# Kernel optimization log

Hardware: AMD Instinct MI355X
Metric: run time of the kernel (lower is better)

Reference implementation:

```python
import jax, jax.numpy as jnp
import numpy as np

B, N, C, H = 8, 1024, 768, 12
D = C // H
SCALE = D ** -0.5


def setup_inputs() -> dict:
    key = jax.random.key(0)
    ks = jax.random.split(key, 6)
    std = 0.02
    return {
        "x": jax.random.normal(ks[0], (B, N, C), dtype=jnp.float32),
        "w_qkv": jax.random.normal(ks[1], (3 * C, C), dtype=jnp.float32) * std,
        "w_proj": jax.random.normal(ks[2], (C, C), dtype=jnp.float32) * std,
        "b_proj": jnp.zeros((C,), dtype=jnp.float32),
        "conv_l_w": jax.random.normal(ks[3], (H, H), dtype=jnp.float32) * std,
        "conv_w_w": jax.random.normal(ks[4], (H, H), dtype=jnp.float32) * std,
    }


def reference(x, w_qkv, w_proj, b_proj, conv_l_w, conv_w_w):
    Bx, Nx, Cx = x.shape
    # qkv projection: torch Linear uses x @ W^T
    qkv = (x @ w_qkv.T).reshape(Bx, Nx, 3, H, D)
    qkv = jnp.transpose(qkv, (2, 0, 3, 1, 4))  # [3, B, H, N, D]
    q, k, v = qkv[0], qkv[1], qkv[2]
    q = q * SCALE
    attn = jnp.einsum("bhnd,bhmd->bhnm", q, k)  # [B,H,N,N]
    # 1x1 conv across heads (conv_l)
    attn = jnp.einsum("oh,bhnm->bonm", conv_l_w, attn)
    attn = jax.nn.softmax(attn, axis=-1)
    # 1x1 conv across heads (conv_w)
    attn = jnp.einsum("oh,bhnm->bonm", conv_w_w, attn)
    out = jnp.einsum("bhnm,bhmd->bhnd", attn, v)
    out = jnp.transpose(out, (0, 2, 1, 3)).reshape(Bx, Nx, Cx)
    return out @ w_proj.T + b_proj
```

## Files before the change

kernel.cpp:

```cpp
#include <hip/hip_runtime.h>
#include <hip/hip_bf16.h>

typedef __attribute__((ext_vector_type(8))) short short8;
typedef __attribute__((ext_vector_type(4))) short short4v;
typedef __attribute__((ext_vector_type(4))) float float4v;

#define NB 8
#define NH 12
#define NN 1024
#define ND 64
#define NC 768

#define RAWBAR() do { \
  asm volatile("s_waitcnt lgkmcnt(0)" ::: "memory"); \
  __builtin_amdgcn_s_barrier(); \
} while (0)

__device__ __forceinline__ short f2bf(float f) {
  __hip_bfloat16 h = __float2bfloat16(f);
  union { __hip_bfloat16 h; short s; } u; u.h = h; return u.s;
}
__device__ __forceinline__ unsigned pk2(float a, float b) {
  unsigned ua = (unsigned short)f2bf(a);
  unsigned ub = (unsigned short)f2bf(b);
  return ua | (ub << 16);
}

template<int MODE>
__global__ __launch_bounds__(256, 2)
void gemm_kernel(const void* __restrict__ Ap, const float* __restrict__ Bw,
                 const float* __restrict__ bias,
                 __hip_bfloat16* __restrict__ Qo, __hip_bfloat16* __restrict__ Ko,
                 __hip_bfloat16* __restrict__ VTo, float* __restrict__ Out)
{
  __shared__ short As[128 * 40];
  __shared__ short Bs[128 * 40];
  const int tid = threadIdx.x;
  const int w = tid >> 6, lane = tid & 63, lr = lane & 15, lg = lane >> 4;
  const int wr = w >> 1, wc = w & 1;
  const int n0 = blockIdx.x * 128, m0 = blockIdx.y * 128;

  float4v acc[4][4];
  #pragma unroll
  for (int i = 0; i < 4; i++)
    #pragma unroll
    for (int j = 0; j < 4; j++)
      acc[i][j] = (float4v){0.f, 0.f, 0.f, 0.f};

  for (int kt = 0; kt < 768; kt += 32) {
    if (MODE == 0) {
      const float* A = (const float*)Ap;
      #pragma unroll
      for (int i2 = 0; i2 < 4; i2++) {
        int c = tid + 256 * i2;
        int row = c >> 3, c4 = c & 7;
        float4v v = *(const float4v*)(A + (size_t)(m0 + row) * 768 + kt + c4 * 4);
        short4v s = { f2bf(v[0]), f2bf(v[1]), f2bf(v[2]), f2bf(v[3]) };
        *(short4v*)(&As[row * 40 + c4 * 4]) = s;
      }
    } else {
      const __hip_bfloat16* A = (const __hip_bfloat16*)Ap;
      #pragma unroll
      for (int i2 = 0; i2 < 2; i2++) {
        int c = tid + 256 * i2;
        int row = c >> 2, c8 = c & 3;
        *(short8*)(&As[row * 40 + c8 * 8]) =
            *(const short8*)(A + (size_t)(m0 + row) * 768 + kt + c8 * 8);
      }
    }
    #pragma unroll
    for (int i2 = 0; i2 < 4; i2++) {
      int c = tid + 256 * i2;
      int row = c >> 3, c4 = c & 7;
      float4v v = *(const float4v*)(Bw + (size_t)(n0 + row) * 768 + kt + c4 * 4);
      short4v s = { f2bf(v[0]), f2bf(v[1]), f2bf(v[2]), f2bf(v[3]) };
      *(short4v*)(&Bs[row * 40 + c4 * 4]) = s;
    }
    __syncthreads();

    short8 af[4], bfr[4];
    #pragma unroll
    for (int i = 0; i < 4; i++)
      af[i] = *(const short8*)(&As[(wr * 64 + i * 16 + lr) * 40 + lg * 8]);
    #pragma unroll
    for (int j = 0; j < 4; j++)
      bfr[j] = *(const short8*)(&Bs[(wc * 64 + j * 16 + lr) * 40 + lg * 8]);
    #pragma unroll
    for (int i = 0; i < 4; i++)
      #pragma unroll
      for (int j = 0; j < 4; j++)
        acc[i][j] = __builtin_amdgcn_mfma_f32_16x16x32_bf16(af[i], bfr[j], acc[i][j], 0, 0, 0);
    __syncthreads();
  }

  #pragma unroll
  for (int i = 0; i < 4; i++) {
    #pragma unroll
    for (int j = 0; j < 4; j++) {
      #pragma unroll
      for (int r = 0; r < 4; r++) {
        float val = acc[i][j][r];
        int mg_ = m0 + wr * 64 + i * 16 + lg * 4 + r;
        int ng_ = n0 + wc * 64 + j * 16 + lr;
        if (MODE == 0) {
          int s = ng_ / 768;
          int rem = ng_ - s * 768;
          int h = rem >> 6, d = rem & 63;
          int b = mg_ >> 10, n = mg_ & 1023;
          if (s == 0)
            Qo[(((size_t)b * NH + h) * NN + n) * ND + d] = __float2bfloat16(val * 0.125f);
          else if (s == 1)
            Ko[(((size_t)b * NH + h) * NN + n) * ND + d] = __float2bfloat16(val);
          else
            VTo[(((size_t)b * NH + h) * ND + d) * NN + n] = __float2bfloat16(val);
        } else {
          Out[(size_t)mg_ * NC + ng_] = val + bias[ng_];
        }
      }
    }
  }
}

__global__ __launch_bounds__(256, 2)
void attn_kernel(const __hip_bfloat16* __restrict__ Qg, const __hip_bfloat16* __restrict__ Kg,
                 const __hip_bfloat16* __restrict__ VTg,
                 const float* __restrict__ convl, const float* __restrict__ convw,
                 __hip_bfloat16* __restrict__ AOut)
{
  __shared__ short Sb[32 * 576];
  __shared__ short pm[16 * 648];
  __shared__ short lwA[512];
  __shared__ short wwT[512];

  const int tid = threadIdx.x;
  const int w = tid >> 6, lane = tid & 63, lr = lane & 15, lg = lane >> 4;
  const int b = blockIdx.x & 7;
  const int n0 = (blockIdx.x >> 3) * 16;
  const float4v zf = (float4v){0.f, 0.f, 0.f, 0.f};

  for (int i = tid; i < 512; i += 256) {
    int r = i >> 5, k = i & 31;
    bool v = (r < 12) && (k < 12);
    lwA[i] = v ? f2bf(convl[r * 12 + k]) : (short)0;
    wwT[i] = v ? f2bf(convw[r * 12 + k]) : (short)0;
  }
  for (int i = tid; i < 512; i += 256) {
    short* p = &Sb[i * 36 + 12];
    #pragma unroll
    for (int j = 0; j < 24; j++) p[j] = 0;
  }

  short8 qf[3][2];
  #pragma unroll
  for (int hh = 0; hh < 3; hh++)
    #pragma unroll
    for (int ks = 0; ks < 2; ks++)
      qf[hh][ks] = *(const short8*)(Qg +
          (((size_t)b * NH + w * 3 + hh) * NN + n0 + lr) * ND + ks * 32 + lg * 8);

  short8 kreg[3][2][2];
  auto loadK = [&](int t) {
    const int m0t = t * 32;
    #pragma unroll
    for (int hh = 0; hh < 3; hh++) {
      const size_t kbase = (((size_t)b * NH + w * 3 + hh) * NN + m0t) * ND;
      #pragma unroll
      for (int j = 0; j < 2; j++)
        #pragma unroll
        for (int ks = 0; ks < 2; ks++)
          kreg[hh][j][ks] = *(const short8*)(Kg + kbase +
              (size_t)(j * 16 + lr) * ND + ks * 32 + lg * 8);
    }
  };
  short8 vt[3][4];
  auto loadVT = [&](int t) {
    const int m0v = t * 32;
    #pragma unroll
    for (int hh = 0; hh < 3; hh++) {
      const size_t vbase = ((size_t)b * NH + w * 3 + hh) * ND * NN;
      #pragma unroll
      for (int jd = 0; jd < 4; jd++)
        vt[hh][jd] = *(const short8*)(VTg + vbase +
            (size_t)(jd * 16 + lr) * NN + m0v + lg * 8);
    }
  };

  loadK(0);
  RAWBAR();
  const short8 lwf = *(const short8*)(&lwA[lr * 32 + lg * 8]);
  const short8 wwf = *(const short8*)(&wwT[lr * 32 + lg * 8]);

  float Lacc[4][4];
  #pragma unroll
  for (int r = 0; r < 4; r++)
    #pragma unroll
    for (int nn = 0; nn < 4; nn++) Lacc[r][nn] = 0.f;

  for (int t = 0; t < 32; t++) {
    __builtin_amdgcn_s_setprio(1);
    #pragma unroll
    for (int hh = 0; hh < 3; hh++) {
      const int h = w * 3 + hh;
      #pragma unroll
      for (int j = 0; j < 2; j++) {
        float4v a = zf;
        #pragma unroll
        for (int ks = 0; ks < 2; ks++)
          a = __builtin_amdgcn_mfma_f32_16x16x32_bf16(qf[hh][ks], kreg[hh][j][ks], a, 0, 0, 0);
        #pragma unroll
        for (int r = 0; r < 4; r++)
          Sb[((lg * 4 + r) * 2 + j) * 576 + lr * 36 + h] = f2bf(a[r]);
      }
    }
    __builtin_amdgcn_s_setprio(0);
    loadK(t < 31 ? t + 1 : 0);
    RAWBAR();
    #pragma unroll
    for (int cc = 0; cc < 8; cc++) {
      const int c = w * 8 + cc;
      short8 sb = *(const short8*)(&Sb[c * 576 + lr * 36 + lg * 8]);
      float4v d = __builtin_amdgcn_mfma_f32_16x16x32_bf16(lwf, sb, zf, 0, 0, 0);
      #pragma unroll
      for (int r = 0; r < 4; r++)
        Lacc[r][cc >> 1] += __expf(d[r]);
    }
    RAWBAR();
  }
  float logLreg[4][4];
  #pragma unroll
  for (int r = 0; r < 4; r++)
    #pragma unroll
    for (int nn = 0; nn < 4; nn++) {
      float v = Lacc[r][nn];
      v += __shfl_xor(v, 1);
      v += __shfl_xor(v, 2);
      v += __shfl_xor(v, 4);
      v += __shfl_xor(v, 8);
      logLreg[r][nn] = __logf(v);
    }

  float4v oacc[3][4];
  #pragma unroll
  for (int hh = 0; hh < 3; hh++)
    #pragma unroll
    for (int jd = 0; jd < 4; jd++) oacc[hh][jd] = zf;

  for (int t = 0; t <= 32; t++) {
    short8 pf[3];
    if (t > 0) {
      #pragma unroll
      for (int hh = 0; hh < 3; hh++)
        pf[hh] = *(const short8*)(&pm[(w * 3 + hh) * 648 + lr * 40 + lg * 8]);
    }
    __builtin_amdgcn_s_setprio(1);
    if (t < 32) {
      #pragma unroll
      for (int hh = 0; hh < 3; hh++) {
        const int h = w * 3 + hh;
        #pragma unroll
        for (int j = 0; j < 2; j++) {
          float4v a = zf;
          #pragma unroll
          for (int ks = 0; ks < 2; ks++)
            a = __builtin_amdgcn_mfma_f32_16x16x32_bf16(qf[hh][ks], kreg[hh][j][ks], a, 0, 0, 0);
          #pragma unroll
          for (int r = 0; r < 4; r++)
            Sb[((lg * 4 + r) * 2 + j) * 576 + lr * 36 + h] = f2bf(a[r]);
        }
      }
      if (t < 31) loadK(t + 1);
    }
    if (t > 0) {
      #pragma unroll
      for (int hh = 0; hh < 3; hh++)
        #pragma unroll
        for (int jd = 0; jd < 4; jd++)
          oacc[hh][jd] = __builtin_amdgcn_mfma_f32_16x16x32_bf16(vt[hh][jd], pf[hh], oacc[hh][jd], 0, 0, 0);
    }
    __builtin_amdgcn_s_setprio(0);
    RAWBAR();
    if (t < 32) {
      loadVT(t);
      #pragma unroll
      for (int cc = 0; cc < 8; cc++) {
        const int c = w * 8 + cc;
        short8 sb = *(const short8*)(&Sb[c * 576 + lr * 36 + lg * 8]);
        float4v d = __builtin_amdgcn_mfma_f32_16x16x32_bf16(lwf, sb, zf, 0, 0, 0);
        float p0 = __expf(d[0] - logLreg[0][cc >> 1]);
        float p1 = __expf(d[1] - logLreg[1][cc >> 1]);
        float p2 = __expf(d[2] - logLreg[2][cc >> 1]);
        float p3 = __expf(d[3] - logLreg[3][cc >> 1]);
        unsigned* dst = (unsigned*)(&Sb[c * 576 + lr * 36 + lg * 4]);
        dst[0] = pk2(p0, p1);
        dst[1] = pk2(p2, p3);
      }
      asm volatile("s_waitcnt lgkmcnt(0)" ::: "memory");
      __builtin_amdgcn_sched_barrier(0);
      #pragma unroll
      for (int cc = 0; cc < 8; cc++) {
        const int c = w * 8 + cc;
        short8 pb = *(const short8*)(&Sb[c * 576 + lr * 36 + lg * 8]);
        float4v d = __builtin_amdgcn_mfma_f32_16x16x32_bf16(pb, wwf, zf, 0, 0, 0);
        unsigned* dst = (unsigned*)(&pm[lr * 648 + (c >> 1) * 40 + (c & 1) * 16 + lg * 4]);
        dst[0] = pk2(d[0], d[1]);
        dst[1] = pk2(d[2], d[3]);
      }
    }
    RAWBAR();
  }

  #pragma unroll
  for (int hh = 0; hh < 3; hh++) {
    const int o2 = w * 3 + hh;
    #pragma unroll
    for (int jd = 0; jd < 4; jd++) {
      size_t base = ((size_t)b * NN + n0 + lr) * NC + o2 * 64 + jd * 16 + lg * 4;
      unsigned* dst = (unsigned*)(&AOut[base]);
      dst[0] = pk2(oacc[hh][jd][0], oacc[hh][jd][1]);
      dst[1] = pk2(oacc[hh][jd][2], oacc[hh][jd][3]);
    }
  }
}

extern "C" void kernel_launch(void* const* d_in, const int* in_sizes, int n_in,
                              void* d_out, int out_size, void* d_ws, size_t ws_size,
                              hipStream_t stream) {
  const float* x      = (const float*)d_in[0];
  const float* w_qkv  = (const float*)d_in[1];
  const float* w_proj = (const float*)d_in[2];
  const float* b_proj = (const float*)d_in[3];
  const float* conv_l = (const float*)d_in[4];
  const float* conv_w = (const float*)d_in[5];
  float* out = (float*)d_out;

  const size_t NE = (size_t)NB * NH * NN * ND;
  __hip_bfloat16* Qb = (__hip_bfloat16*)d_ws;
  __hip_bfloat16* Kb = Qb + NE;
  __hip_bfloat16* VT = Kb + NE;
  __hip_bfloat16* AO = VT + NE;

  gemm_kernel<0><<<dim3(18, 64), 256, 0, stream>>>(x, w_qkv, nullptr, Qb, Kb, VT, nullptr);
  attn_kernel<<<dim3(512), 256, 0, stream>>>(Qb, Kb, VT, conv_l, conv_w, AO);
  gemm_kernel<1><<<dim3(6, 64), 256, 0, stream>>>(AO, w_proj, b_proj, nullptr, nullptr, nullptr, out);
}
```

Measured before the change: 375.5 us.

## Split attention work across 8 waves and swizzle score buffer in LDS

The attention kernel grows from 4 to 8 wavefronts per block. Each wave now owns three (head, key-half) units instead of three whole heads, which halves per-wave registers for K, V^T and the output accumulators. The padded score buffer becomes a compact 32-byte-stride layout with an XOR swizzle to avoid LDS bank conflicts, shrinking LDS use. V^T loads move into the consumer step and are issued right before use. More waves should improve latency hiding, at the cost of more barrier participants and V loads that are no longer prefetched a step ahead.

```diff
diff --git a/kernel.cpp b/kernel.cpp
--- a/kernel.cpp
+++ b/kernel.cpp
@@ -15,6 +15,8 @@
   asm volatile("s_waitcnt lgkmcnt(0)" ::: "memory"); \
   __builtin_amdgcn_s_barrier(); \
 } while (0)
+
+#define SWZ(byt) ((byt) ^ (((((byt) >> 5) ^ ((byt) >> 12)) & 7) << 4))
 
 __device__ __forceinline__ short f2bf(float f) {
   __hip_bfloat16 h = __float2bfloat16(f);
@@ -121,67 +123,56 @@
   }
 }
 
-__global__ __launch_bounds__(256, 2)
+__global__ __launch_bounds__(512, 4)
 void attn_kernel(const __hip_bfloat16* __restrict__ Qg, const __hip_bfloat16* __restrict__ Kg,
                  const __hip_bfloat16* __restrict__ VTg,
                  const float* __restrict__ convl, const float* __restrict__ convw,
                  __hip_bfloat16* __restrict__ AOut)
 {
-  __shared__ short Sb[32 * 576];
+  __shared__ short Sb[8256];
   __shared__ short pm[16 * 648];
   __shared__ short lwA[512];
   __shared__ short wwT[512];
 
+  char* Sbb = (char*)Sb;
   const int tid = threadIdx.x;
   const int w = tid >> 6, lane = tid & 63, lr = lane & 15, lg = lane >> 4;
   const int b = blockIdx.x & 7;
   const int n0 = (blockIdx.x >> 3) * 16;
+  const int u0 = w * 3;
+  const int h0 = u0 >> 1;
   const float4v zf = (float4v){0.f, 0.f, 0.f, 0.f};
 
-  for (int i = tid; i < 512; i += 256) {
+  for (int i = tid; i < 512; i += 512) {
     int r = i >> 5, k = i & 31;
     bool v = (r < 12) && (k < 12);
     lwA[i] = v ? f2bf(convl[r * 12 + k]) : (short)0;
     wwT[i] = v ? f2bf(convw[r * 12 + k]) : (short)0;
   }
-  for (int i = tid; i < 512; i += 256) {
-    short* p = &Sb[i * 36 + 12];
-    #pragma unroll
-    for (int j = 0; j < 24; j++) p[j] = 0;
-  }
-
-  short8 qf[3][2];
-  #pragma unroll
-  for (int hh = 0; hh < 3; hh++)
+  {
+    int chunk = tid >> 4, col = tid & 15;
+    *(int*)(Sbb + SWZ(chunk * 512 + col * 32 + 24)) = 0;
+    *(int*)(Sbb + SWZ(chunk * 512 + col * 32 + 28)) = 0;
+    if (tid < 32) *(int*)(Sbb + 16384 + tid * 4) = 0;
+  }
+
+  short8 qf[2][2];
+  #pragma unroll
+  for (int hi = 0; hi < 2; hi++)
     #pragma unroll
     for (int ks = 0; ks < 2; ks++)
-      qf[hh][ks] = *(const short8*)(Qg +
-          (((size_t)b * NH + w * 3 + hh) * NN + n0 + lr) * ND + ks * 32 + lg * 8);
-
-  short8 kreg[3][2][2];
+      qf[hi][ks] = *(const short8*)(Qg +
+          (((size_t)b * NH + h0 + hi) * NN + n0 + lr) * ND + ks * 32 + lg * 8);
+
+  short8 kreg[3][2];
   auto loadK = [&](int t) {
-    const int m0t = t * 32;
-    #pragma unroll
-    for (int hh = 0; hh < 3; hh++) {
-      const size_t kbase = (((size_t)b * NH + w * 3 + hh) * NN + m0t) * ND;
-      #pragma unroll
-      for (int j = 0; j < 2; j++)
-        #pragma unroll
-        for (int ks = 0; ks < 2; ks++)
-          kreg[hh][j][ks] = *(const short8*)(Kg + kbase +
-              (size_t)(j * 16 + lr) * ND + ks * 32 + lg * 8);
-    }
-  };
-  short8 vt[3][4];
-  auto loadVT = [&](int t) {
-    const int m0v = t * 32;
-    #pragma unroll
-    for (int hh = 0; hh < 3; hh++) {
-      const size_t vbase = ((size_t)b * NH + w * 3 + hh) * ND * NN;
-      #pragma unroll
-      for (int jd = 0; jd < 4; jd++)
-        vt[hh][jd] = *(const short8*)(VTg + vbase +
-            (size_t)(jd * 16 + lr) * NN + m0v + lg * 8);
+    #pragma unroll
+    for (int uu = 0; uu < 3; uu++) {
+      int u = u0 + uu, h = u >> 1, j = u & 1;
+      const size_t kbase = (((size_t)b * NH + h) * NN + t * 32 + j * 16 + lr) * ND;
+      #pragma unroll
+      for (int ks = 0; ks < 2; ks++)
+        kreg[uu][ks] = *(const short8*)(Kg + kbase + ks * 32 + lg * 8);
     }
   };
 
@@ -190,35 +181,28 @@
   const short8 lwf = *(const short8*)(&lwA[lr * 32 + lg * 8]);
   const short8 wwf = *(const short8*)(&wwT[lr * 32 + lg * 8]);
 
-  float Lacc[4][4];
-  #pragma unroll
-  for (int r = 0; r < 4; r++)
-    #pragma unroll
-    for (int nn = 0; nn < 4; nn++) Lacc[r][nn] = 0.f;
+  float Lacc[4][2];
+  #pragma unroll
+  for (int r = 0; r < 4; r++) { Lacc[r][0] = 0.f; Lacc[r][1] = 0.f; }
 
   for (int t = 0; t < 32; t++) {
     __builtin_amdgcn_s_setprio(1);
     #pragma unroll
-    for (int hh = 0; hh < 3; hh++) {
-      const int h = w * 3 + hh;
-      #pragma unroll
-      for (int j = 0; j < 2; j++) {
-        float4v a = zf;
-        #pragma unroll
-        for (int ks = 0; ks < 2; ks++)
-          a = __builtin_amdgcn_mfma_f32_16x16x32_bf16(qf[hh][ks], kreg[hh][j][ks], a, 0, 0, 0);
-        #pragma unroll
-        for (int r = 0; r < 4; r++)
-          Sb[((lg * 4 + r) * 2 + j) * 576 + lr * 36 + h] = f2bf(a[r]);
-      }
+    for (int uu = 0; uu < 3; uu++) {
+      int u = u0 + uu, h = u >> 1, j = u & 1, hi = h - h0;
+      float4v a = __builtin_amdgcn_mfma_f32_16x16x32_bf16(qf[hi][0], kreg[uu][0], zf, 0, 0, 0);
+      a = __builtin_amdgcn_mfma_f32_16x16x32_bf16(qf[hi][1], kreg[uu][1], a, 0, 0, 0);
+      #pragma unroll
+      for (int r = 0; r < 4; r++)
+        *(short*)(Sbb + SWZ((((lg * 4 + r) * 2 + j) * 512) + lr * 32 + h * 2)) = f2bf(a[r]);
     }
     __builtin_amdgcn_s_setprio(0);
     loadK(t < 31 ? t + 1 : 0);
     RAWBAR();
     #pragma unroll
-    for (int cc = 0; cc < 8; cc++) {
-      const int c = w * 8 + cc;
-      short8 sb = *(const short8*)(&Sb[c * 576 + lr * 36 + lg * 8]);
+    for (int cc = 0; cc < 4; cc++) {
+      const int c = w * 4 + cc;
+      short8 sb = *(const short8*)(Sbb + SWZ(c * 512 + lr * 32 + lg * 16));
       float4v d = __builtin_amdgcn_mfma_f32_16x16x32_bf16(lwf, sb, zf, 0, 0, 0);
       #pragma unroll
       for (int r = 0; r < 4; r++)
@@ -226,11 +210,11 @@
     }
     RAWBAR();
   }
-  float logLreg[4][4];
+  float logLreg[4][2];
   #pragma unroll
   for (int r = 0; r < 4; r++)
     #pragma unroll
-    for (int nn = 0; nn < 4; nn++) {
+    for (int nn = 0; nn < 2; nn++) {
       float v = Lacc[r][nn];
       v += __shfl_xor(v, 1);
       v += __shfl_xor(v, 2);
@@ -239,67 +223,67 @@
       logLreg[r][nn] = __logf(v);
     }
 
-  float4v oacc[3][4];
-  #pragma unroll
-  for (int hh = 0; hh < 3; hh++)
-    #pragma unroll
-    for (int jd = 0; jd < 4; jd++) oacc[hh][jd] = zf;
+  float4v oacc[3][2];
+  #pragma unroll
+  for (int uu = 0; uu < 3; uu++) { oacc[uu][0] = zf; oacc[uu][1] = zf; }
 
   for (int t = 0; t <= 32; t++) {
     short8 pf[3];
+    short8 vt[3][2];
     if (t > 0) {
-      #pragma unroll
-      for (int hh = 0; hh < 3; hh++)
-        pf[hh] = *(const short8*)(&pm[(w * 3 + hh) * 648 + lr * 40 + lg * 8]);
+      const int m0v = (t - 1) * 32;
+      #pragma unroll
+      for (int uu = 0; uu < 3; uu++) {
+        int u = u0 + uu, o2v = u >> 1, jdp = u & 1;
+        pf[uu] = *(const short8*)(&pm[o2v * 648 + lr * 40 + lg * 8]);
+        const size_t vbase = ((size_t)b * NH + o2v) * ND * NN;
+        #pragma unroll
+        for (int q = 0; q < 2; q++)
+          vt[uu][q] = *(const short8*)(VTg + vbase +
+              (size_t)((jdp * 2 + q) * 16 + lr) * NN + m0v + lg * 8);
+      }
     }
     __builtin_amdgcn_s_setprio(1);
     if (t < 32) {
       #pragma unroll
-      for (int hh = 0; hh < 3; hh++) {
-        const int h = w * 3 + hh;
+      for (int uu = 0; uu < 3; uu++) {
+        int u = u0 + uu, h = u >> 1, j = u & 1, hi = h - h0;
+        float4v a = __builtin_amdgcn_mfma_f32_16x16x32_bf16(qf[hi][0], kreg[uu][0], zf, 0, 0, 0);
+        a = __builtin_amdgcn_mfma_f32_16x16x32_bf16(qf[hi][1], kreg[uu][1], a, 0, 0, 0);
         #pragma unroll
-        for (int j = 0; j < 2; j++) {
-          float4v a = zf;
-          #pragma unroll
-          for (int ks = 0; ks < 2; ks++)
-            a = __builtin_amdgcn_mfma_f32_16x16x32_bf16(qf[hh][ks], kreg[hh][j][ks], a, 0, 0, 0);
-          #pragma unroll
-          for (int r = 0; r < 4; r++)
-            Sb[((lg * 4 + r) * 2 + j) * 576 + lr * 36 + h] = f2bf(a[r]);
-        }
+        for (int r = 0; r < 4; r++)
+          *(short*)(Sbb + SWZ((((lg * 4 + r) * 2 + j) * 512) + lr * 32 + h * 2)) = f2bf(a[r]);
       }
       if (t < 31) loadK(t + 1);
     }
     if (t > 0) {
       #pragma unroll
-      for (int hh = 0; hh < 3; hh++)
+      for (int uu = 0; uu < 3; uu++)
         #pragma unroll
-        for (int jd = 0; jd < 4; jd++)
-          oacc[hh][jd] = __builtin_amdgcn_mfma_f32_16x16x32_bf16(vt[hh][jd], pf[hh], oacc[hh][jd], 0, 0, 0);
+        for (int q = 0; q < 2; q++)
+          oacc[uu][q] = __builtin_amdgcn_mfma_f32_16x16x32_bf16(vt[uu][q], pf[uu], oacc[uu][q], 0, 0, 0);
     }
     __builtin_amdgcn_s_setprio(0);
     RAWBAR();
     if (t < 32) {
-      loadVT(t);
-      #pragma unroll
-      for (int cc = 0; cc < 8; cc++) {
-        const int c = w * 8 + cc;
-        short8 sb = *(const short8*)(&Sb[c * 576 + lr * 36 + lg * 8]);
+      #pragma unroll
+      for (int cc = 0; cc < 4; cc++) {
+        const int c = w * 4 + cc;
+        short8 sb = *(const short8*)(Sbb + SWZ(c * 512 + lr * 32 + lg * 16));
         float4v d = __builtin_amdgcn_mfma_f32_16x16x32_bf16(lwf, sb, zf, 0, 0, 0);
         float p0 = __expf(d[0] - logLreg[0][cc >> 1]);
         float p1 = __expf(d[1] - logLreg[1][cc >> 1]);
         float p2 = __expf(d[2] - logLreg[2][cc >> 1]);
         float p3 = __expf(d[3] - logLreg[3][cc >> 1]);
-        unsigned* dst = (unsigned*)(&Sb[c * 576 + lr * 36 + lg * 4]);
-        dst[0] = pk2(p0, p1);
-        dst[1] = pk2(p2, p3);
+        *(unsigned*)(Sbb + SWZ(c * 512 + lr * 32 + lg * 8)) = pk2(p0, p1);
+        *(unsigned*)(Sbb + SWZ(c * 512 + lr * 32 + lg * 8 + 4)) = pk2(p2, p3);
       }
       asm volatile("s_waitcnt lgkmcnt(0)" ::: "memory");
       __builtin_amdgcn_sched_barrier(0);
       #pragma unroll
-      for (int cc = 0; cc < 8; cc++) {
-        const int c = w * 8 + cc;
-        short8 pb = *(const short8*)(&Sb[c * 576 + lr * 36 + lg * 8]);
+      for (int cc = 0; cc < 4; cc++) {
+        const int c = w * 4 + cc;
+        short8 pb = *(const short8*)(Sbb + SWZ(c * 512 + lr * 32 + lg * 16));
         float4v d = __builtin_amdgcn_mfma_f32_16x16x32_bf16(pb, wwf, zf, 0, 0, 0);
         unsigned* dst = (unsigned*)(&pm[lr * 648 + (c >> 1) * 40 + (c & 1) * 16 + lg * 4]);
         dst[0] = pk2(d[0], d[1]);
@@ -310,14 +294,14 @@
   }
 
   #pragma unroll
-  for (int hh = 0; hh < 3; hh++) {
-    const int o2 = w * 3 + hh;
-    #pragma unroll
-    for (int jd = 0; jd < 4; jd++) {
-      size_t base = ((size_t)b * NN + n0 + lr) * NC + o2 * 64 + jd * 16 + lg * 4;
+  for (int uu = 0; uu < 3; uu++) {
+    int u = u0 + uu, o2v = u >> 1, jdp = u & 1;
+    #pragma unroll
+    for (int q = 0; q < 2; q++) {
+      size_t base = ((size_t)b * NN + n0 + lr) * NC + o2v * 64 + jdp * 32 + q * 16 + lg * 4;
       unsigned* dst = (unsigned*)(&AOut[base]);
-      dst[0] = pk2(oacc[hh][jd][0], oacc[hh][jd][1]);
-      dst[1] = pk2(oacc[hh][jd][2], oacc[hh][jd][3]);
+      dst[0] = pk2(oacc[uu][q][0], oacc[uu][q][1]);
+      dst[1] = pk2(oacc[uu][q][2], oacc[uu][q][3]);
     }
   }
 }
@@ -340,6 +324,6 @@
   __hip_bfloat16* AO = VT + NE;
 
   gemm_kernel<0><<<dim3(18, 64), 256, 0, stream>>>(x, w_qkv, nullptr, Qb, Kb, VT, nullptr);
-  attn_kernel<<<dim3(512), 256, 0, stream>>>(Qb, Kb, VT, conv_l, conv_w, AO);
+  attn_kernel<<<dim3(512), 512, 0, stream>>>(Qb, Kb, VT, conv_l, conv_w, AO);
   gemm_kernel<1><<<dim3(6, 64), 256, 0, stream>>>(AO, w_proj, b_proj, nullptr, nullptr, nullptr, out);
 }
```

New measurement: 674.9 us. +79.7%, slower.

## Double-buffer score and probability LDS tiles to drop one barrier per step

Applied to the files above, without the earlier changes.

Sb and pm become double-buffered with tighter strides (18 and 584/36 instead of 36 and 648/40). QK^T for tile t is written to one buffer while the conv/exp work for tile t-1 reads the other. This removes one of the two barriers per iteration and deepens the pipeline to three stages, with the PV MFMA lagging two tiles. V^T loads move next to the PV step, and LDS use grows, which may limit the 2-blocks-per-CU occupancy target.

```diff
diff --git a/kernel.cpp b/kernel.cpp
--- a/kernel.cpp
+++ b/kernel.cpp
@@ -127,8 +127,8 @@
                  const float* __restrict__ convl, const float* __restrict__ convw,
                  __hip_bfloat16* __restrict__ AOut)
 {
-  __shared__ short Sb[32 * 576];
-  __shared__ short pm[16 * 648];
+  __shared__ short Sb[18432];
+  __shared__ short pm[18688];
   __shared__ short lwA[512];
   __shared__ short wwT[512];
 
@@ -144,10 +144,9 @@
     lwA[i] = v ? f2bf(convl[r * 12 + k]) : (short)0;
     wwT[i] = v ? f2bf(convw[r * 12 + k]) : (short)0;
   }
-  for (int i = tid; i < 512; i += 256) {
-    short* p = &Sb[i * 36 + 12];
-    #pragma unroll
-    for (int j = 0; j < 24; j++) p[j] = 0;
+  for (int i = tid; i < 1024; i += 256) {
+    unsigned* p = (unsigned*)(&Sb[i * 18 + 12]);
+    p[0] = 0; p[1] = 0; p[2] = 0;
   }
 
   short8 qf[3][2];
@@ -160,10 +159,9 @@
 
   short8 kreg[3][2][2];
   auto loadK = [&](int t) {
-    const int m0t = t * 32;
     #pragma unroll
     for (int hh = 0; hh < 3; hh++) {
-      const size_t kbase = (((size_t)b * NH + w * 3 + hh) * NN + m0t) * ND;
+      const size_t kbase = (((size_t)b * NH + w * 3 + hh) * NN + t * 32) * ND;
       #pragma unroll
       for (int j = 0; j < 2; j++)
         #pragma unroll
@@ -172,16 +170,19 @@
               (size_t)(j * 16 + lr) * ND + ks * 32 + lg * 8);
     }
   };
-  short8 vt[3][4];
-  auto loadVT = [&](int t) {
-    const int m0v = t * 32;
+
+  auto qkStep = [&](int buf) {
     #pragma unroll
     for (int hh = 0; hh < 3; hh++) {
-      const size_t vbase = ((size_t)b * NH + w * 3 + hh) * ND * NN;
-      #pragma unroll
-      for (int jd = 0; jd < 4; jd++)
-        vt[hh][jd] = *(const short8*)(VTg + vbase +
-            (size_t)(jd * 16 + lr) * NN + m0v + lg * 8);
+      const int h = w * 3 + hh;
+      #pragma unroll
+      for (int j = 0; j < 2; j++) {
+        float4v a = __builtin_amdgcn_mfma_f32_16x16x32_bf16(qf[hh][0], kreg[hh][j][0], zf, 0, 0, 0);
+        a = __builtin_amdgcn_mfma_f32_16x16x32_bf16(qf[hh][1], kreg[hh][j][1], a, 0, 0, 0);
+        #pragma unroll
+        for (int r = 0; r < 4; r++)
+          Sb[(buf * 32 + (lg * 4 + r) * 2 + j) * 288 + lr * 18 + h] = f2bf(a[r]);
+      }
     }
   };
 
@@ -196,33 +197,22 @@
     #pragma unroll
     for (int nn = 0; nn < 4; nn++) Lacc[r][nn] = 0.f;
 
-  for (int t = 0; t < 32; t++) {
+  for (int t = 0; t <= 32; t++) {
     __builtin_amdgcn_s_setprio(1);
-    #pragma unroll
-    for (int hh = 0; hh < 3; hh++) {
-      const int h = w * 3 + hh;
-      #pragma unroll
-      for (int j = 0; j < 2; j++) {
-        float4v a = zf;
-        #pragma unroll
-        for (int ks = 0; ks < 2; ks++)
-          a = __builtin_amdgcn_mfma_f32_16x16x32_bf16(qf[hh][ks], kreg[hh][j][ks], a, 0, 0, 0);
+    if (t < 32) qkStep(t & 1);
+    __builtin_amdgcn_s_setprio(0);
+    if (t < 32) loadK(t < 31 ? t + 1 : 0);
+    if (t >= 1) {
+      const int buf = (t - 1) & 1;
+      #pragma unroll
+      for (int cc = 0; cc < 8; cc++) {
+        const int c = w * 8 + cc;
+        short8 sb = *(const short8*)(&Sb[(buf * 32 + c) * 288 + lr * 18 + lg * 8]);
+        float4v d = __builtin_amdgcn_mfma_f32_16x16x32_bf16(lwf, sb, zf, 0, 0, 0);
         #pragma unroll
         for (int r = 0; r < 4; r++)
-          Sb[((lg * 4 + r) * 2 + j) * 576 + lr * 36 + h] = f2bf(a[r]);
-      }
-    }
-    __builtin_amdgcn_s_setprio(0);
-    loadK(t < 31 ? t + 1 : 0);
-    RAWBAR();
-    #pragma unroll
-    for (int cc = 0; cc < 8; cc++) {
-      const int c = w * 8 + cc;
-      short8 sb = *(const short8*)(&Sb[c * 576 + lr * 36 + lg * 8]);
-      float4v d = __builtin_amdgcn_mfma_f32_16x16x32_bf16(lwf, sb, zf, 0, 0, 0);
-      #pragma unroll
-      for (int r = 0; r < 4; r++)
-        Lacc[r][cc >> 1] += __expf(d[r]);
+          Lacc[r][cc >> 1] += __expf(d[r]);
+      }
     }
     RAWBAR();
   }
@@ -245,52 +235,41 @@
     #pragma unroll
     for (int jd = 0; jd < 4; jd++) oacc[hh][jd] = zf;
 
-  for (int t = 0; t <= 32; t++) {
+  for (int t = 0; t <= 33; t++) {
     short8 pf[3];
-    if (t > 0) {
-      #pragma unroll
-      for (int hh = 0; hh < 3; hh++)
-        pf[hh] = *(const short8*)(&pm[(w * 3 + hh) * 648 + lr * 40 + lg * 8]);
+    short8 vt[3][4];
+    if (t >= 2) {
+      const int pb = t & 1;
+      const int m0v = (t - 2) * 32;
+      #pragma unroll
+      for (int hh = 0; hh < 3; hh++) {
+        const int o2 = w * 3 + hh;
+        pf[hh] = *(const short8*)(&pm[pb * 9344 + o2 * 584 + lr * 36 + lg * 8]);
+        const size_t vbase = ((size_t)b * NH + o2) * ND * NN;
+        #pragma unroll
+        for (int jd = 0; jd < 4; jd++)
+          vt[hh][jd] = *(const short8*)(VTg + vbase +
+              (size_t)(jd * 16 + lr) * NN + m0v + lg * 8);
+      }
     }
     __builtin_amdgcn_s_setprio(1);
     if (t < 32) {
-      #pragma unroll
-      for (int hh = 0; hh < 3; hh++) {
-        const int h = w * 3 + hh;
-        #pragma unroll
-        for (int j = 0; j < 2; j++) {
-          float4v a = zf;
-          #pragma unroll
-          for (int ks = 0; ks < 2; ks++)
-            a = __builtin_amdgcn_mfma_f32_16x16x32_bf16(qf[hh][ks], kreg[hh][j][ks], a, 0, 0, 0);
-          #pragma unroll
-          for (int r = 0; r < 4; r++)
-            Sb[((lg * 4 + r) * 2 + j) * 576 + lr * 36 + h] = f2bf(a[r]);
-        }
-      }
+      qkStep(t & 1);
       if (t < 31) loadK(t + 1);
     }
-    if (t > 0) {
-      #pragma unroll
-      for (int hh = 0; hh < 3; hh++)
-        #pragma unroll
-        for (int jd = 0; jd < 4; jd++)
-          oacc[hh][jd] = __builtin_amdgcn_mfma_f32_16x16x32_bf16(vt[hh][jd], pf[hh], oacc[hh][jd], 0, 0, 0);
-    }
     __builtin_amdgcn_s_setprio(0);
-    RAWBAR();
-    if (t < 32) {
-      loadVT(t);
+    if (t >= 1 && t <= 32) {
+      const int buf = (t - 1) & 1;
       #pragma unroll
       for (int cc = 0; cc < 8; cc++) {
         const int c = w * 8 + cc;
-        short8 sb = *(const short8*)(&Sb[c * 576 + lr * 36 + lg * 8]);
+        short8 sb = *(const short8*)(&Sb[(buf * 32 + c) * 288 + lr * 18 + lg * 8]);
         float4v d = __builtin_amdgcn_mfma_f32_16x16x32_bf16(lwf, sb, zf, 0, 0, 0);
         float p0 = __expf(d[0] - logLreg[0][cc >> 1]);
         float p1 = __expf(d[1] - logLreg[1][cc >> 1]);
         float p2 = __expf(d[2] - logLreg[2][cc >> 1]);
         float p3 = __expf(d[3] - logLreg[3][cc >> 1]);
-        unsigned* dst = (unsigned*)(&Sb[c * 576 + lr * 36 + lg * 4]);
+        unsigned* dst = (unsigned*)(&Sb[(buf * 32 + c) * 288 + lr * 18 + lg * 4]);
         dst[0] = pk2(p0, p1);
         dst[1] = pk2(p2, p3);
       }
@@ -299,12 +278,21 @@
       #pragma unroll
       for (int cc = 0; cc < 8; cc++) {
         const int c = w * 8 + cc;
-        short8 pb = *(const short8*)(&Sb[c * 576 + lr * 36 + lg * 8]);
-        float4v d = __builtin_amdgcn_mfma_f32_16x16x32_bf16(pb, wwf, zf, 0, 0, 0);
-        unsigned* dst = (unsigned*)(&pm[lr * 648 + (c >> 1) * 40 + (c & 1) * 16 + lg * 4]);
+        short8 pb2 = *(const short8*)(&Sb[(buf * 32 + c) * 288 + lr * 18 + lg * 8]);
+        float4v d = __builtin_amdgcn_mfma_f32_16x16x32_bf16(pb2, wwf, zf, 0, 0, 0);
+        unsigned* dst = (unsigned*)(&pm[buf * 9344 + lr * 584 + (c >> 1) * 36 + (c & 1) * 16 + lg * 4]);
         dst[0] = pk2(d[0], d[1]);
         dst[1] = pk2(d[2], d[3]);
       }
+    }
+    if (t >= 2) {
+      __builtin_amdgcn_s_setprio(1);
+      #pragma unroll
+      for (int hh = 0; hh < 3; hh++)
+        #pragma unroll
+        for (int jd = 0; jd < 4; jd++)
+          oacc[hh][jd] = __builtin_amdgcn_mfma_f32_16x16x32_bf16(vt[hh][jd], pf[hh], oacc[hh][jd], 0, 0, 0);
+      __builtin_amdgcn_s_setprio(0);
     }
     RAWBAR();
   }
```

New measurement: 377.0 us. No clear change (+0.4%).

## Split attention into L-sum and PV kernels with key-dimension halving

Applied to the files above, without the earlier changes.

The fused attention kernel becomes two kernels plus a reduction. The first computes the softmax denominators and the second the probability-times-V products, each splitting the key range into two halves so the grid doubles to 1024 blocks. Each block streams K/V straight from global memory instead of prefetching into registers, and shared-memory padding is reduced to raise occupancy. A separate add kernel sums the two partial outputs and writes them in token-major layout. The cost is recomputing QK^T in both passes, extra global traffic for the partial outputs, and two additional launches.

```diff
diff --git a/kernel.cpp b/kernel.cpp
--- a/kernel.cpp
+++ b/kernel.cpp
@@ -19,6 +19,9 @@
 __device__ __forceinline__ short f2bf(float f) {
   __hip_bfloat16 h = __float2bfloat16(f);
   union { __hip_bfloat16 h; short s; } u; u.h = h; return u.s;
+}
+__device__ __forceinline__ float bf2f(short s) {
+  union { float f; unsigned u; } u; u.u = ((unsigned)(unsigned short)s) << 16; return u.f;
 }
 __device__ __forceinline__ unsigned pk2(float a, float b) {
   unsigned ua = (unsigned short)f2bf(a);
@@ -121,34 +124,25 @@
   }
 }
 
-__global__ __launch_bounds__(256, 2)
-void attn_kernel(const __hip_bfloat16* __restrict__ Qg, const __hip_bfloat16* __restrict__ Kg,
-                 const __hip_bfloat16* __restrict__ VTg,
-                 const float* __restrict__ convl, const float* __restrict__ convw,
-                 __hip_bfloat16* __restrict__ AOut)
+__global__ __launch_bounds__(256, 4)
+void attn_l_kernel(const __hip_bfloat16* __restrict__ Qg, const __hip_bfloat16* __restrict__ Kg,
+                   const float* __restrict__ convl, float* __restrict__ Lg)
 {
-  __shared__ short Sb[32 * 576];
-  __shared__ short pm[16 * 648];
+  __shared__ short Sb[2 * 9408];
   __shared__ short lwA[512];
-  __shared__ short wwT[512];
-
   const int tid = threadIdx.x;
   const int w = tid >> 6, lane = tid & 63, lr = lane & 15, lg = lane >> 4;
   const int b = blockIdx.x & 7;
-  const int n0 = (blockIdx.x >> 3) * 16;
+  const int rest = blockIdx.x >> 3;
+  const int n0 = (rest >> 1) * 16;
+  const int mh = rest & 1;
   const float4v zf = (float4v){0.f, 0.f, 0.f, 0.f};
 
   for (int i = tid; i < 512; i += 256) {
     int r = i >> 5, k = i & 31;
-    bool v = (r < 12) && (k < 12);
-    lwA[i] = v ? f2bf(convl[r * 12 + k]) : (short)0;
-    wwT[i] = v ? f2bf(convw[r * 12 + k]) : (short)0;
-  }
-  for (int i = tid; i < 512; i += 256) {
-    short* p = &Sb[i * 36 + 12];
-    #pragma unroll
-    for (int j = 0; j < 24; j++) p[j] = 0;
-  }
+    lwA[i] = (r < 12 && k < 12) ? f2bf(convl[r * 12 + k]) : (short)0;
+  }
+  for (int i = tid; i < 9408; i += 256) ((unsigned*)Sb)[i] = 0u;
 
   short8 qf[3][2];
   #pragma unroll
@@ -157,38 +151,8 @@
     for (int ks = 0; ks < 2; ks++)
       qf[hh][ks] = *(const short8*)(Qg +
           (((size_t)b * NH + w * 3 + hh) * NN + n0 + lr) * ND + ks * 32 + lg * 8);
-
-  short8 kreg[3][2][2];
-  auto loadK = [&](int t) {
-    const int m0t = t * 32;
-    #pragma unroll
-    for (int hh = 0; hh < 3; hh++) {
-      const size_t kbase = (((size_t)b * NH + w * 3 + hh) * NN + m0t) * ND;
-      #pragma unroll
-      for (int j = 0; j < 2; j++)
-        #pragma unroll
-        for (int ks = 0; ks < 2; ks++)
-          kreg[hh][j][ks] = *(const short8*)(Kg + kbase +
-              (size_t)(j * 16 + lr) * ND + ks * 32 + lg * 8);
-    }
-  };
-  short8 vt[3][4];
-  auto loadVT = [&](int t) {
-    const int m0v = t * 32;
-    #pragma unroll
-    for (int hh = 0; hh < 3; hh++) {
-      const size_t vbase = ((size_t)b * NH + w * 3 + hh) * ND * NN;
-      #pragma unroll
-      for (int jd = 0; jd < 4; jd++)
-        vt[hh][jd] = *(const short8*)(VTg + vbase +
-            (size_t)(jd * 16 + lr) * NN + m0v + lg * 8);
-    }
-  };
-
-  loadK(0);
   RAWBAR();
   const short8 lwf = *(const short8*)(&lwA[lr * 32 + lg * 8]);
-  const short8 wwf = *(const short8*)(&wwT[lr * 32 + lg * 8]);
 
   float Lacc[4][4];
   #pragma unroll
@@ -196,37 +160,43 @@
     #pragma unroll
     for (int nn = 0; nn < 4; nn++) Lacc[r][nn] = 0.f;
 
-  for (int t = 0; t < 32; t++) {
+  for (int t = 0; t <= 16; t++) {
     __builtin_amdgcn_s_setprio(1);
-    #pragma unroll
-    for (int hh = 0; hh < 3; hh++) {
-      const int h = w * 3 + hh;
-      #pragma unroll
-      for (int j = 0; j < 2; j++) {
-        float4v a = zf;
+    if (t < 16) {
+      const int m0t = (mh * 16 + t) * 32;
+      const int buf = (t & 1) * 9408;
+      #pragma unroll
+      for (int hh = 0; hh < 3; hh++) {
+        const int h = w * 3 + hh;
+        const size_t kbase = (((size_t)b * NH + h) * NN + m0t) * ND;
         #pragma unroll
-        for (int ks = 0; ks < 2; ks++)
-          a = __builtin_amdgcn_mfma_f32_16x16x32_bf16(qf[hh][ks], kreg[hh][j][ks], a, 0, 0, 0);
+        for (int j = 0; j < 2; j++) {
+          short8 kb0 = *(const short8*)(Kg + kbase + (size_t)(j * 16 + lr) * ND + lg * 8);
+          short8 kb1 = *(const short8*)(Kg + kbase + (size_t)(j * 16 + lr) * ND + 32 + lg * 8);
+          float4v a = __builtin_amdgcn_mfma_f32_16x16x32_bf16(qf[hh][0], kb0, zf, 0, 0, 0);
+          a = __builtin_amdgcn_mfma_f32_16x16x32_bf16(qf[hh][1], kb1, a, 0, 0, 0);
+          #pragma unroll
+          for (int r = 0; r < 4; r++)
+            Sb[buf + ((lg * 4 + r) * 2 + j) * 292 + lr * 18 + h] = f2bf(a[r]);
+        }
+      }
+    }
+    __builtin_amdgcn_s_setprio(0);
+    if (t >= 1) {
+      const int buf = ((t - 1) & 1) * 9408;
+      #pragma unroll
+      for (int cc = 0; cc < 8; cc++) {
+        const int c = w * 8 + cc;
+        short8 sb = *(const short8*)(&Sb[buf + c * 292 + lr * 18 + lg * 8]);
+        float4v d = __builtin_amdgcn_mfma_f32_16x16x32_bf16(lwf, sb, zf, 0, 0, 0);
         #pragma unroll
         for (int r = 0; r < 4; r++)
-          Sb[((lg * 4 + r) * 2 + j) * 576 + lr * 36 + h] = f2bf(a[r]);
-      }
-    }
-    __builtin_amdgcn_s_setprio(0);
-    loadK(t < 31 ? t + 1 : 0);
+          Lacc[r][cc >> 1] += __expf(d[r]);
+      }
+    }
     RAWBAR();
-    #pragma unroll
-    for (int cc = 0; cc < 8; cc++) {
-      const int c = w * 8 + cc;
-      short8 sb = *(const short8*)(&Sb[c * 576 + lr * 36 + lg * 8]);
-      float4v d = __builtin_amdgcn_mfma_f32_16x16x32_bf16(lwf, sb, zf, 0, 0, 0);
-      #pragma unroll
-      for (int r = 0; r < 4; r++)
-        Lacc[r][cc >> 1] += __expf(d[r]);
-    }
-    RAWBAR();
-  }
-  float logLreg[4][4];
+  }
+
   #pragma unroll
   for (int r = 0; r < 4; r++)
     #pragma unroll
@@ -236,8 +206,64 @@
       v += __shfl_xor(v, 2);
       v += __shfl_xor(v, 4);
       v += __shfl_xor(v, 8);
-      logLreg[r][nn] = __logf(v);
-    }
+      int o = lg * 4 + r;
+      if (lr == 0 && o < 12)
+        Lg[((size_t)(mh * 8 + b) * NH + o) * NN + n0 + w * 4 + nn] = v;
+    }
+}
+
+__global__ __launch_bounds__(256, 3)
+void attn_pv_kernel(const __hip_bfloat16* __restrict__ Qg, const __hip_bfloat16* __restrict__ Kg,
+                    const __hip_bfloat16* __restrict__ VTg,
+                    const float* __restrict__ convl, const float* __restrict__ convw,
+                    const float* __restrict__ Lg, __hip_bfloat16* __restrict__ Ug)
+{
+  __shared__ short Sb[9408];
+  __shared__ short pm[9344];
+  __shared__ short lwA[512];
+  __shared__ short wwT[512];
+  __shared__ float invLs[256];
+
+  const int tid = threadIdx.x;
+  const int w = tid >> 6, lane = tid & 63, lr = lane & 15, lg = lane >> 4;
+  const int b = blockIdx.x & 7;
+  const int rest = blockIdx.x >> 3;
+  const int n0 = (rest >> 1) * 16;
+  const int mh = rest & 1;
+  const float4v zf = (float4v){0.f, 0.f, 0.f, 0.f};
+
+  for (int i = tid; i < 512; i += 256) {
+    int r = i >> 5, k = i & 31;
+    bool v = (r < 12) && (k < 12);
+    lwA[i] = v ? f2bf(convl[r * 12 + k]) : (short)0;
+    wwT[i] = v ? f2bf(convw[r * 12 + k]) : (short)0;
+  }
+  for (int i = tid; i < 4704; i += 256) ((unsigned*)Sb)[i] = 0u;
+  if (tid < 192) {
+    int o = tid >> 4, nl = tid & 15;
+    float l = Lg[((size_t)b * NH + o) * NN + n0 + nl] +
+              Lg[((size_t)(8 + b) * NH + o) * NN + n0 + nl];
+    invLs[tid] = 1.0f / l;
+  } else if (tid < 256) {
+    invLs[tid] = 0.f;
+  }
+
+  short8 qf[3][2];
+  #pragma unroll
+  for (int hh = 0; hh < 3; hh++)
+    #pragma unroll
+    for (int ks = 0; ks < 2; ks++)
+      qf[hh][ks] = *(const short8*)(Qg +
+          (((size_t)b * NH + w * 3 + hh) * NN + n0 + lr) * ND + ks * 32 + lg * 8);
+  RAWBAR();
+  const short8 lwf = *(const short8*)(&lwA[lr * 32 + lg * 8]);
+  const short8 wwf = *(const short8*)(&wwT[lr * 32 + lg * 8]);
+  float invLreg[4][4];
+  #pragma unroll
+  for (int r = 0; r < 4; r++)
+    #pragma unroll
+    for (int nn = 0; nn < 4; nn++)
+      invLreg[r][nn] = invLs[(lg * 4 + r) * 16 + w * 4 + nn];
 
   float4v oacc[3][4];
   #pragma unroll
@@ -245,52 +271,59 @@
     #pragma unroll
     for (int jd = 0; jd < 4; jd++) oacc[hh][jd] = zf;
 
-  for (int t = 0; t <= 32; t++) {
+  for (int t = 0; t <= 16; t++) {
     short8 pf[3];
     if (t > 0) {
       #pragma unroll
       for (int hh = 0; hh < 3; hh++)
-        pf[hh] = *(const short8*)(&pm[(w * 3 + hh) * 648 + lr * 40 + lg * 8]);
+        pf[hh] = *(const short8*)(&pm[(w * 3 + hh) * 584 + lr * 36 + lg * 8]);
     }
     __builtin_amdgcn_s_setprio(1);
-    if (t < 32) {
+    if (t < 16) {
+      const int m0t = (mh * 16 + t) * 32;
       #pragma unroll
       for (int hh = 0; hh < 3; hh++) {
         const int h = w * 3 + hh;
+        const size_t kbase = (((size_t)b * NH + h) * NN + m0t) * ND;
         #pragma unroll
         for (int j = 0; j < 2; j++) {
-          float4v a = zf;
-          #pragma unroll
-          for (int ks = 0; ks < 2; ks++)
-            a = __builtin_amdgcn_mfma_f32_16x16x32_bf16(qf[hh][ks], kreg[hh][j][ks], a, 0, 0, 0);
+          short8 kb0 = *(const short8*)(Kg + kbase + (size_t)(j * 16 + lr) * ND + lg * 8);
+          short8 kb1 = *(const short8*)(Kg + kbase + (size_t)(j * 16 + lr) * ND + 32 + lg * 8);
+          float4v a = __builtin_amdgcn_mfma_f32_16x16x32_bf16(qf[hh][0], kb0, zf, 0, 0, 0);
+          a = __builtin_amdgcn_mfma_f32_16x16x32_bf16(qf[hh][1], kb1, a, 0, 0, 0);
           #pragma unroll
           for (int r = 0; r < 4; r++)
-            Sb[((lg * 4 + r) * 2 + j) * 576 + lr * 36 + h] = f2bf(a[r]);
+            Sb[((lg * 4 + r) * 2 + j) * 292 + lr * 18 + h] = f2bf(a[r]);
         }
       }
-      if (t < 31) loadK(t + 1);
     }
     if (t > 0) {
-      #pragma unroll
-      for (int hh = 0; hh < 3; hh++)
+      const int m0v = (mh * 16 + t - 1) * 32;
+      #pragma unroll
+      for (int jd = 0; jd < 4; jd++) {
+        short8 vt[3];
         #pragma unroll
-        for (int jd = 0; jd < 4; jd++)
-          oacc[hh][jd] = __builtin_amdgcn_mfma_f32_16x16x32_bf16(vt[hh][jd], pf[hh], oacc[hh][jd], 0, 0, 0);
+        for (int hh = 0; hh < 3; hh++)
+          vt[hh] = *(const short8*)(VTg +
+              (((size_t)b * NH + w * 3 + hh) * ND + jd * 16 + lr) * NN + m0v + lg * 8);
+        #pragma unroll
+        for (int hh = 0; hh < 3; hh++)
+          oacc[hh][jd] = __builtin_amdgcn_mfma_f32_16x16x32_bf16(vt[hh], pf[hh], oacc[hh][jd], 0, 0, 0);
+      }
     }
     __builtin_amdgcn_s_setprio(0);
     RAWBAR();
-    if (t < 32) {
-      loadVT(t);
+    if (t < 16) {
       #pragma unroll
       for (int cc = 0; cc < 8; cc++) {
         const int c = w * 8 + cc;
-        short8 sb = *(const short8*)(&Sb[c * 576 + lr * 36 + lg * 8]);
+        short8 sb = *(const short8*)(&Sb[c * 292 + lr * 18 + lg * 8]);
         float4v d = __builtin_amdgcn_mfma_f32_16x16x32_bf16(lwf, sb, zf, 0, 0, 0);
-        float p0 = __expf(d[0] - logLreg[0][cc >> 1]);
-        float p1 = __expf(d[1] - logLreg[1][cc >> 1]);
-        float p2 = __expf(d[2] - logLreg[2][cc >> 1]);
-        float p3 = __expf(d[3] - logLreg[3][cc >> 1]);
-        unsigned* dst = (unsigned*)(&Sb[c * 576 + lr * 36 + lg * 4]);
+        float p0 = __expf(d[0]) * invLreg[0][cc >> 1];
+        float p1 = __expf(d[1]) * invLreg[1][cc >> 1];
+        float p2 = __expf(d[2]) * invLreg[2][cc >> 1];
+        float p3 = __expf(d[3]) * invLreg[3][cc >> 1];
+        unsigned* dst = (unsigned*)(&Sb[c * 292 + lr * 18 + lg * 4]);
         dst[0] = pk2(p0, p1);
         dst[1] = pk2(p2, p3);
       }
@@ -299,9 +332,9 @@
       #pragma unroll
       for (int cc = 0; cc < 8; cc++) {
         const int c = w * 8 + cc;
-        short8 pb = *(const short8*)(&Sb[c * 576 + lr * 36 + lg * 8]);
-        float4v d = __builtin_amdgcn_mfma_f32_16x16x32_bf16(pb, wwf, zf, 0, 0, 0);
-        unsigned* dst = (unsigned*)(&pm[lr * 648 + (c >> 1) * 40 + (c & 1) * 16 + lg * 4]);
+        short8 pb2 = *(const short8*)(&Sb[c * 292 + lr * 18 + lg * 8]);
+        float4v d = __builtin_amdgcn_mfma_f32_16x16x32_bf16(pb2, wwf, zf, 0, 0, 0);
+        unsigned* dst = (unsigned*)(&pm[lr * 584 + (c >> 1) * 36 + (c & 1) * 16 + lg * 4]);
         dst[0] = pk2(d[0], d[1]);
         dst[1] = pk2(d[2], d[3]);
       }
@@ -314,11 +347,33 @@
     const int o2 = w * 3 + hh;
     #pragma unroll
     for (int jd = 0; jd < 4; jd++) {
-      size_t base = ((size_t)b * NN + n0 + lr) * NC + o2 * 64 + jd * 16 + lg * 4;
-      unsigned* dst = (unsigned*)(&AOut[base]);
+      size_t base = (((size_t)(mh * 8 + b) * NH + o2) * NN + n0 + lr) * ND + jd * 16 + lg * 4;
+      unsigned* dst = (unsigned*)(&Ug[base]);
       dst[0] = pk2(oacc[hh][jd][0], oacc[hh][jd][1]);
       dst[1] = pk2(oacc[hh][jd][2], oacc[hh][jd][3]);
     }
+  }
+}
+
+__global__ __launch_bounds__(256)
+void add_kernel(const __hip_bfloat16* __restrict__ Ug, __hip_bfloat16* __restrict__ AOut)
+{
+  const size_t NE = (size_t)NB * NH * NN * ND;
+  const unsigned* U0 = (const unsigned*)Ug;
+  const unsigned* U1 = (const unsigned*)(Ug + NE);
+  for (size_t i = (size_t)blockIdx.x * 256 + threadIdx.x; i < NE / 2;
+       i += (size_t)gridDim.x * 256) {
+    unsigned a = U0[i], c = U1[i];
+    size_t e = i << 1;
+    int d = (int)(e & 63);
+    size_t r1 = e >> 6;
+    int n = (int)(r1 & 1023);
+    size_t r2 = r1 >> 10;
+    int o2 = (int)(r2 % 12);
+    int b = (int)(r2 / 12);
+    float s0 = bf2f((short)(a & 0xffff)) + bf2f((short)(c & 0xffff));
+    float s1 = bf2f((short)(a >> 16)) + bf2f((short)(c >> 16));
+    *(unsigned*)(&AOut[((size_t)b * NN + n) * NC + o2 * 64 + d]) = pk2(s0, s1);
   }
 }
 
@@ -337,9 +392,13 @@
   __hip_bfloat16* Qb = (__hip_bfloat16*)d_ws;
   __hip_bfloat16* Kb = Qb + NE;
   __hip_bfloat16* VT = Kb + NE;
-  __hip_bfloat16* AO = VT + NE;
+  __hip_bfloat16* Ug = VT + NE;
+  __hip_bfloat16* AO = Ug + 2 * NE;
+  float* Lg = (float*)(AO + NE);
 
   gemm_kernel<0><<<dim3(18, 64), 256, 0, stream>>>(x, w_qkv, nullptr, Qb, Kb, VT, nullptr);
-  attn_kernel<<<dim3(512), 256, 0, stream>>>(Qb, Kb, VT, conv_l, conv_w, AO);
+  attn_l_kernel<<<dim3(1024), 256, 0, stream>>>(Qb, Kb, conv_l, Lg);
+  attn_pv_kernel<<<dim3(1024), 256, 0, stream>>>(Qb, Kb, VT, conv_l, conv_w, Lg, Ug);
+  add_kernel<<<dim3(2048), 256, 0, stream>>>(Ug, AO);
   gemm_kernel<1><<<dim3(6, 64), 256, 0, stream>>>(AO, w_proj, b_proj, nullptr, nullptr, nullptr, out);
 }
```

After: 500.5 us. +33.3%, slower.
